# Kernel tuning notes

Measured on AMD Instinct MI355X. Metric: run time of the kernel, lower is better.

## Reference

```python
import jax, jax.numpy as jnp
import numpy as np

N_GROUPS = 32
EPS = 1e-6


def group_norm(x, gamma, beta):
    # x: (b, c, h, w); 32 groups, eps=1e-6, affine
    b, c, h, w = x.shape
    xg = x.reshape(b, N_GROUPS, c // N_GROUPS, h, w)
    mean = xg.mean(axis=(2, 3, 4), keepdims=True)
    var = xg.var(axis=(2, 3, 4), keepdims=True)
    xg = (xg - mean) * jax.lax.rsqrt(var + EPS)
    x = xg.reshape(b, c, h, w)
    return x * gamma[None, :, None, None] + beta[None, :, None, None]


def setup_inputs() -> dict:
    key = jax.random.key(0)
    ks = jax.random.split(key, 8)
    b, c, h, w = 4, 512, 64, 64
    sc = 1.0 / np.sqrt(c)
    return {
        "x": jax.random.normal(ks[0], (b, c, h, w), jnp.float32),
        "gn_w": jnp.ones((c,), jnp.float32),
        "gn_b": jnp.zeros((c,), jnp.float32),
        "wq": jax.random.normal(ks[1], (c, c), jnp.float32) * sc,
        "bq": jnp.zeros((c,), jnp.float32),
        "wk": jax.random.normal(ks[2], (c, c), jnp.float32) * sc,
        "bk": jnp.zeros((c,), jnp.float32),
        "wv": jax.random.normal(ks[3], (c, c), jnp.float32) * sc,
        "bv": jnp.zeros((c,), jnp.float32),
        "wo": jax.random.normal(ks[4], (c, c), jnp.float32) * sc,
        "bo": jnp.zeros((c,), jnp.float32),
    }


def reference(x, gn_w, gn_b, wq, bq, wk, bk, wv, bv, wo, bo):
    b, c, h, w = x.shape
    s = c ** (-0.5)
    xn = group_norm(x, gn_w, gn_b)
    xf = xn.reshape(b, c, h * w)  # (b, c, hw)
    # 1x1 convs == channel matmuls: weight (out_c, in_c)
    q = jnp.einsum('oc,bci->boi', wq, xf) + bq[None, :, None]
    k = jnp.einsum('oc,bci->boi', wk, xf) + bk[None, :, None]
    v = jnp.einsum('oc,bci->boi', wv, xf) + bv[None, :, None]
    attn = jnp.einsum('bci,bcj->bij', q, k) * s  # (b, hw, hw)
    attn = jax.nn.softmax(attn, axis=-1)
    out = jnp.einsum('bij,bcj->bci', attn, v)  # (b, c, hw)
    out = jnp.einsum('oc,bci->boi', wo, out) + bo[None, :, None]
    return out.reshape(b, c, h, w) + x
```

## Files before the change

### kernel.cpp

```cpp
#include <hip/hip_runtime.h>

#define B 4
#define C 512
#define HW 4096
#define NG 32
#define GSZ 65536
#define KROW 528

typedef unsigned short u16;
typedef unsigned int u32;
typedef __attribute__((ext_vector_type(8))) short short8;
typedef __attribute__((ext_vector_type(4))) float f32x4;

__device__ __forceinline__ u16 f2bf(float f) {
    union { u32 i; float f; } x; x.f = f;
    u32 r = x.i + 0x7FFF + ((x.i >> 16) & 1);
    return (u16)(r >> 16);
}
__device__ __forceinline__ u32 cvtpk(float lo, float hi) {
    u32 r;
    asm("v_cvt_pk_bf16_f32 %0, %1, %2" : "=v"(r) : "v"(lo), "v"(hi));
    return r;
}

__device__ __forceinline__ void gld16(const u16* g, u16* l) {
    __builtin_amdgcn_global_load_lds(
        (const __attribute__((address_space(1))) void*)g,
        (__attribute__((address_space(3))) void*)l, 16, 0, 0);
}

__global__ __launch_bounds__(256) void prep_kernel(
        const float* __restrict__ wq, const float* __restrict__ wk,
        const float* __restrict__ wv, const float* __restrict__ wo,
        u16* __restrict__ dst, const float* __restrict__ x,
        float2* __restrict__ part) {
    const int bid = blockIdx.x;
    const int tid = threadIdx.x;
    if (bid < 1024) {
        const int mat = bid >> 8;
        const float* src = (mat == 0) ? wq : (mat == 1) ? wk : (mat == 2) ? wv : wo;
        const int idx = ((bid & 255) * 256 + tid) * 4;
        float4 v = *(const float4*)(src + idx);
        uint2 r = make_uint2(cvtpk(v.x, v.y), cvtpk(v.z, v.w));
        *(uint2*)(dst + (size_t)mat * (C * C) + idx) = r;
        return;
    }
    const int idx2 = bid - 1024;
    const int gl = idx2 >> 2;
    const int qt = idx2 & 3;
    const size_t base = (size_t)gl * GSZ + (size_t)qt * (GSZ / 4);
    float s = 0.f, s2 = 0.f;
    for (int i = tid * 4; i < GSZ / 4; i += 1024) {
        float4 v4 = *(const float4*)(x + base + i);
        s  += v4.x + v4.y + v4.z + v4.w;
        s2 += v4.x*v4.x + v4.y*v4.y + v4.z*v4.z + v4.w*v4.w;
    }
    #pragma unroll
    for (int off = 32; off > 0; off >>= 1) {
        s  += __shfl_down(s, off, 64);
        s2 += __shfl_down(s2, off, 64);
    }
    __shared__ float rs[4], rs2[4];
    int lane = tid & 63, wid = tid >> 6;
    if (lane == 0) { rs[wid] = s; rs2[wid] = s2; }
    __syncthreads();
    if (tid == 0) {
        part[gl * 4 + qt] = make_float2(rs[0] + rs[1] + rs[2] + rs[3],
                                        rs2[0] + rs2[1] + rs2[2] + rs2[3]);
    }
}

__global__ __launch_bounds__(256) void gn_apply_kernel(
        const float* __restrict__ x, const float* __restrict__ gamma,
        const float* __restrict__ beta, const float2* __restrict__ part,
        u16* __restrict__ xnT) {
    const int b = blockIdx.y;
    const int i0 = blockIdx.x * 32;
    const int tid = threadIdx.x;
    __shared__ float gm[512], bt[512];
    __shared__ __align__(16) u16 tile[32 * 512];

    for (int c = tid; c < 512; c += 256) {
        int g = c >> 4;
        const float2* pp = part + ((size_t)b * 32 + g) * 4;
        float2 p0 = pp[0], p1 = pp[1], p2 = pp[2], p3 = pp[3];
        float mean = (p0.x + p1.x + p2.x + p3.x) * (1.f / GSZ);
        float var  = (p0.y + p1.y + p2.y + p3.y) * (1.f / GSZ) - mean * mean;
        float rstd = rsqrtf(var + 1e-6f);
        float gg = gamma[c] * rstd;
        gm[c] = gg;
        bt[c] = beta[c] - mean * gg;
    }
    __syncthreads();
    const int ci = tid >> 5;
    const int ii = tid & 31;
    const float* xb = x + (size_t)b * 512 * 4096 + i0;
    #pragma unroll 4
    for (int p = 0; p < 64; p++) {
        int c = p * 8 + ci;
        float v = xb[(size_t)c * 4096 + ii] * gm[c] + bt[c];
        tile[ii * 512 + (c ^ ((ii & 7) << 3))] = f2bf(v);
    }
    __syncthreads();
    u16* dst = xnT + ((size_t)b * HW + i0) * C;
    #pragma unroll
    for (int p = 0; p < 8; p++) {
        int i = p * 4 + (tid >> 6);
        int ch = tid & 63;
        *(uint4*)(dst + (size_t)i * C + ch * 8) =
            *(const uint4*)&tile[i * 512 + ((ch ^ (i & 7)) << 3)];
    }
}

__global__ __launch_bounds__(256) void qkv_kernel(
        const u16* __restrict__ xnT, const u16* __restrict__ wb,
        const float* __restrict__ bq, const float* __restrict__ bk,
        const float* __restrict__ bv,
        u16* __restrict__ qT, u16* __restrict__ kT, u16* __restrict__ vimg) {
    const int mat = blockIdx.y >> 2;
    const int oT0 = (blockIdx.y & 3) * 128;
    const int iT0 = blockIdx.x * 128;
    const int b = blockIdx.z;
    const u16* Ag = xnT + ((size_t)b * HW + iT0) * C;
    const u16* Bg = wb + (size_t)mat * C * C + (size_t)oT0 * C;
    const float* bias = (mat == 0) ? bq : (mat == 1) ? bk : bv;

    const int tid = threadIdx.x;
    const int w = tid >> 6, lane = tid & 63;
    const int qd = lane >> 4, nn = lane & 15;
    const int wm = w & 1, wn = w >> 1;

    __shared__ __align__(16) u16 smem[16384];
    u16* As0 = smem;
    u16* Bs0 = smem + 8192;

    f32x4 acc[4][4];
    #pragma unroll
    for (int mt = 0; mt < 4; mt++)
        #pragma unroll
        for (int nt = 0; nt < 4; nt++) acc[mt][nt] = (f32x4){0.f, 0.f, 0.f, 0.f};

    auto stage = [&](u16* dst, const u16* g, int c0) {
        #pragma unroll
        for (int p = 0; p < 2; p++) {
            int rbase = 32 * w + 16 * p;
            int row = rbase + (lane >> 2);
            gld16(g + (size_t)row * C + c0 + (((lane & 3) ^ ((row >> 1) & 3)) << 3),
                  dst + rbase * 32);
        }
    };

    stage(As0, Ag, 0);
    stage(Bs0, Bg, 0);

    for (int kt = 0; kt < 16; kt++) {
        const int cur = kt & 1;
        __syncthreads();
        if (kt < 15) {
            stage(As0 + (cur ^ 1) * 4096, Ag, (kt + 1) * 32);
            stage(Bs0 + (cur ^ 1) * 4096, Bg, (kt + 1) * 32);
        }
        const u16* Ac = As0 + cur * 4096;
        const u16* Bc = Bs0 + cur * 4096;
        short8 af[4], bf[4];
        #pragma unroll
        for (int mt = 0; mt < 4; mt++) {
            int row = 64 * wm + 16 * mt + nn;
            af[mt] = *(const short8*)&Ac[row * 32 + ((qd ^ ((row >> 1) & 3)) << 3)];
        }
        #pragma unroll
        for (int nt = 0; nt < 4; nt++) {
            int row = 64 * wn + 16 * nt + nn;
            bf[nt] = *(const short8*)&Bc[row * 32 + ((qd ^ ((row >> 1) & 3)) << 3)];
        }
        #pragma unroll
        for (int mt = 0; mt < 4; mt++)
            #pragma unroll
            for (int nt = 0; nt < 4; nt++)
                acc[mt][nt] = __builtin_amdgcn_mfma_f32_16x16x32_bf16(af[mt], bf[nt], acc[mt][nt], 0, 0, 0);
    }

    __syncthreads();
    u16* dt = smem;

    if (mat < 2) {
        #pragma unroll
        for (int nt = 0; nt < 4; nt++) {
            int o_l = 64 * wn + 16 * nt + nn;
            float bb = bias[oT0 + o_l];
            #pragma unroll
            for (int mt = 0; mt < 4; mt++) {
                int i_l = 64 * wm + 16 * mt + qd * 4;
                dt[(i_l + 0) * 128 + o_l] = f2bf(acc[mt][nt][0] + bb);
                dt[(i_l + 1) * 128 + o_l] = f2bf(acc[mt][nt][1] + bb);
                dt[(i_l + 2) * 128 + o_l] = f2bf(acc[mt][nt][2] + bb);
                dt[(i_l + 3) * 128 + o_l] = f2bf(acc[mt][nt][3] + bb);
            }
        }
        __syncthreads();
        u16* dstT = ((mat == 0) ? qT : kT) + ((size_t)b * HW + iT0) * C + oT0;
        #pragma unroll
        for (int p = 0; p < 8; p++) {
            int i_l = p * 16 + (tid >> 4);
            int ch = tid & 15;
            *(uint4*)(dstT + (size_t)i_l * C + ch * 8) = *(const uint4*)&dt[i_l * 128 + ch * 8];
        }
    } else {
        #pragma unroll
        for (int nt = 0; nt < 4; nt++) {
            int c_l = 64 * wn + 16 * nt + nn;
            float bb = bias[oT0 + c_l];
            #pragma unroll
            for (int mt = 0; mt < 4; mt++) {
                int i_l = 64 * wm + 16 * mt + qd * 4;
                int lc = i_l >> 5;
                int j0 = i_l & 31;
                union { uint2 u; ushort4 s; } st;
                st.u = make_uint2(cvtpk(acc[mt][nt][0] + bb, acc[mt][nt][1] + bb),
                                  cvtpk(acc[mt][nt][2] + bb, acc[mt][nt][3] + bb));
                *(ushort4*)&dt[lc * 4096 + c_l * 32 +
                               (((j0 >> 3) ^ ((c_l >> 2) & 3)) << 3) + (j0 & 7)] = st.s;
            }
        }
        __syncthreads();
        u16* vb = vimg + (size_t)b * 128 * 16384;
        const int chb = iT0 >> 5;
        #pragma unroll
        for (int p = 0; p < 8; p++) {
            int lc = p >> 1, half = p & 1;
            *(uint4*)(vb + (size_t)(chb + lc) * 16384 + oT0 * 32 + half * 2048 + tid * 8) =
                *(const uint4*)&dt[lc * 4096 + half * 2048 + tid * 8];
        }
    }
}

__global__ __launch_bounds__(512, 2) void attn_kernel(
        const u16* __restrict__ qT, const u16* __restrict__ kT,
        const u16* __restrict__ vimg, u16* __restrict__ oT) {
    const int b = blockIdx.y;
    const int i0 = blockIdx.x * 64;
    const int tid = threadIdx.x;
    const int w = tid >> 6;
    const int lane = tid & 63;
    const int q = lane >> 4;
    const int n = lane & 15;
    const int rw = w & 3;
    const int jh = w >> 2;

    __shared__ __align__(16) u16 kbuf[2][32 * KROW];
    __shared__ __align__(16) u16 pbuf[2][64 * 40];
    __shared__ __align__(16) float lpart[2][64];

    short8 qf[16];
    {
        const u16* qrow = qT + ((size_t)b * HW + i0 + rw * 16 + n) * C + q * 8;
        #pragma unroll
        for (int k = 0; k < 16; k++) {
            uint4 u = *(const uint4*)(qrow + k * 32);
            qf[k] = *(const short8*)&u;
        }
    }
    f32x4 oacc[4][4];
    #pragma unroll
    for (int mt = 0; mt < 4; mt++)
        #pragma unroll
        for (int ct = 0; ct < 4; ct++)
            oacc[mt][ct] = (f32x4){0.f, 0.f, 0.f, 0.f};
    float lsum[4] = {0.f, 0.f, 0.f, 0.f};

    const u16* kTb = kT + (size_t)b * HW * C;
    const u16* vTb = vimg + (size_t)b * 128 * 16384;

    auto stageK = [&](int gc, int buf) {
        const u16* gk = kTb + (size_t)gc * 32 * C;
        #pragma unroll
        for (int ii = 0; ii < 4; ii++) {
            int j = w * 4 + ii;
            gld16(gk + (size_t)j * C + ((lane ^ (j & 7)) << 3), &kbuf[buf][j * KROW]);
        }
    };

    const float scale = 0.04419417382415922f;
    stageK(0, 0);
    stageK(1, 1);
    __syncthreads();

    auto s_phase = [&](int slot, int par) {
        f32x4 s0 = {0.f,0.f,0.f,0.f}, s1 = {0.f,0.f,0.f,0.f};
        f32x4 s2 = {0.f,0.f,0.f,0.f}, s3 = {0.f,0.f,0.f,0.f};
        const int sw = n & 7;
        const u16* kb = kbuf[slot] + (jh * 16 + n) * KROW;
        __builtin_amdgcn_s_setprio(1);
        #pragma unroll
        for (int m = 0; m < 4; m++) {
            short8 b0 = *(const short8*)&kb[(((4 * m + 0) * 4 + q) ^ sw) << 3];
            short8 b1 = *(const short8*)&kb[(((4 * m + 1) * 4 + q) ^ sw) << 3];
            short8 b2 = *(const short8*)&kb[(((4 * m + 2) * 4 + q) ^ sw) << 3];
            short8 b3 = *(const short8*)&kb[(((4 * m + 3) * 4 + q) ^ sw) << 3];
            s0 = __builtin_amdgcn_mfma_f32_16x16x32_bf16(qf[4 * m + 0], b0, s0, 0, 0, 0);
            s1 = __builtin_amdgcn_mfma_f32_16x16x32_bf16(qf[4 * m + 1], b1, s1, 0, 0, 0);
            s2 = __builtin_amdgcn_mfma_f32_16x16x32_bf16(qf[4 * m + 2], b2, s2, 0, 0, 0);
            s3 = __builtin_amdgcn_mfma_f32_16x16x32_bf16(qf[4 * m + 3], b3, s3, 0, 0, 0);
        }
        __builtin_amdgcn_s_setprio(0);
        float sv[4];
        #pragma unroll
        for (int r = 0; r < 4; r++) sv[r] = ((s0[r] + s1[r]) + (s2[r] + s3[r])) * scale;
        float p0 = __expf(sv[0]), p1 = __expf(sv[1]);
        float p2 = __expf(sv[2]), p3 = __expf(sv[3]);
        lsum[0] += p0;
        lsum[1] += p1;
        lsum[2] += p2;
        lsum[3] += p3;
        u32 a = cvtpk(p0, p1), c = cvtpk(p2, p3);
        u16* pb = &pbuf[par][(rw * 16 + q * 4) * 40 + jh * 16 + n];
        pb[0]      = (u16)a;
        pb[40]     = (u16)(a >> 16);
        pb[80]     = (u16)c;
        pb[120]    = (u16)(c >> 16);
    };

    s_phase(0, 0);
    __syncthreads();

    #pragma unroll 1
    for (int t = 0; t < 128; ++t) {
        const int cur = t & 1;
        short8 pf[4];
        #pragma unroll
        for (int mt = 0; mt < 4; mt++)
            pf[mt] = *(const short8*)&pbuf[cur][(mt * 16 + n) * 40 + q * 8];
        uint4 vpf[4];
        {
            const u16* gv = vTb + (size_t)t * 16384;
            #pragma unroll
            for (int ct = 0; ct < 4; ct++) {
                int c = w * 64 + ct * 16 + n;
                vpf[ct] = *(const uint4*)&gv[c * 32 + ((q ^ ((c >> 2) & 3)) << 3)];
            }
        }
        if (t < 126) stageK(t + 2, cur);
        if (t < 127) s_phase(cur ^ 1, cur ^ 1);
        __builtin_amdgcn_s_setprio(1);
        #pragma unroll
        for (int ct = 0; ct < 4; ct++) {
            short8 vf = *(const short8*)&vpf[ct];
            #pragma unroll
            for (int mt = 0; mt < 4; mt++)
                oacc[mt][ct] = __builtin_amdgcn_mfma_f32_16x16x32_bf16(pf[mt], vf, oacc[mt][ct], 0, 0, 0);
        }
        __builtin_amdgcn_s_setprio(0);
        __syncthreads();
    }
    #pragma unroll
    for (int r = 0; r < 4; r++) {
        float l = lsum[r];
        l += __shfl_xor(l, 1);
        l += __shfl_xor(l, 2);
        l += __shfl_xor(l, 4);
        l += __shfl_xor(l, 8);
        if (n == 0) lpart[jh][rw * 16 + q * 4 + r] = l;
    }
    __syncthreads();
    #pragma unroll
    for (int mt = 0; mt < 4; mt++) {
        float inv[4];
        #pragma unroll
        for (int r = 0; r < 4; r++) {
            int row = mt * 16 + q * 4 + r;
            inv[r] = 1.f / (lpart[0][row] + lpart[1][row]);
        }
        #pragma unroll
        for (int ct = 0; ct < 4; ct++) {
            int cc = w * 64 + ct * 16 + n;
            size_t base = ((size_t)b * HW + i0 + mt * 16 + q * 4) * C + cc;
            oT[base        ] = f2bf(oacc[mt][ct][0] * inv[0]);
            oT[base +   C  ] = f2bf(oacc[mt][ct][1] * inv[1]);
            oT[base + 2 * C] = f2bf(oacc[mt][ct][2] * inv[2]);
            oT[base + 3 * C] = f2bf(oacc[mt][ct][3] * inv[3]);
        }
    }
}

__global__ __launch_bounds__(256) void proj_kernel(
        const u16* __restrict__ oT, const u16* __restrict__ wob,
        const float* __restrict__ bo, const float* __restrict__ x,
        float* __restrict__ out) {
    const int o0 = blockIdx.y * 128;
    const int i0t = blockIdx.x * 128;
    const int b = blockIdx.z;
    const u16* Ag = wob + (size_t)o0 * C;
    const u16* Bg = oT + ((size_t)b * HW + i0t) * C;

    const int tid = threadIdx.x;
    const int w = tid >> 6, lane = tid & 63;
    const int qd = lane >> 4, nn = lane & 15;
    const int wm = w & 1, wn = w >> 1;

    __shared__ __align__(16) u16 As[2][128 * 32];
    __shared__ __align__(16) u16 Bs[2][128 * 32];

    f32x4 acc[4][4];
    #pragma unroll
    for (int mt = 0; mt < 4; mt++)
        #pragma unroll
        for (int nt = 0; nt < 4; nt++) acc[mt][nt] = (f32x4){0.f, 0.f, 0.f, 0.f};

    auto stage = [&](u16* dst, const u16* g, int c0) {
        #pragma unroll
        for (int p = 0; p < 2; p++) {
            int rbase = 32 * w + 16 * p;
            int row = rbase + (lane >> 2);
            gld16(g + (size_t)row * C + c0 + (((lane & 3) ^ ((row >> 1) & 3)) << 3),
                  dst + rbase * 32);
        }
    };

    stage(As[0], Ag, 0);
    stage(Bs[0], Bg, 0);

    for (int kt = 0; kt < 16; kt++) {
        const int cur = kt & 1;
        __syncthreads();
        if (kt < 15) {
            stage(As[cur ^ 1], Ag, (kt + 1) * 32);
            stage(Bs[cur ^ 1], Bg, (kt + 1) * 32);
        }
        short8 af[4], bf[4];
        #pragma unroll
        for (int mt = 0; mt < 4; mt++) {
            int row = 64 * wm + 16 * mt + nn;
            af[mt] = *(const short8*)&As[cur][row * 32 + ((qd ^ ((row >> 1) & 3)) << 3)];
        }
        #pragma unroll
        for (int nt = 0; nt < 4; nt++) {
            int row = 64 * wn + 16 * nt + nn;
            bf[nt] = *(const short8*)&Bs[cur][row * 32 + ((qd ^ ((row >> 1) & 3)) << 3)];
        }
        #pragma unroll
        for (int mt = 0; mt < 4; mt++)
            #pragma unroll
            for (int nt = 0; nt < 4; nt++)
                acc[mt][nt] = __builtin_amdgcn_mfma_f32_16x16x32_bf16(af[mt], bf[nt], acc[mt][nt], 0, 0, 0);
    }

    #pragma unroll
    for (int mt = 0; mt < 4; mt++) {
        #pragma unroll
        for (int r = 0; r < 4; r++) {
            int o = o0 + 64 * wm + 16 * mt + qd * 4 + r;
            float bb = bo[o];
            #pragma unroll
            for (int nt = 0; nt < 4; nt++) {
                int i = i0t + 64 * wn + 16 * nt + nn;
                size_t idx = ((size_t)b * C + o) * HW + i;
                out[idx] = acc[mt][nt][r] + bb + x[idx];
            }
        }
    }
}

extern "C" void kernel_launch(void* const* d_in, const int* in_sizes, int n_in,
                              void* d_out, int out_size, void* d_ws, size_t ws_size,
                              hipStream_t stream) {
    const float* x    = (const float*)d_in[0];
    const float* gn_w = (const float*)d_in[1];
    const float* gn_b = (const float*)d_in[2];
    const float* wq   = (const float*)d_in[3];
    const float* bq   = (const float*)d_in[4];
    const float* wk   = (const float*)d_in[5];
    const float* bk   = (const float*)d_in[6];
    const float* wv   = (const float*)d_in[7];
    const float* bv   = (const float*)d_in[8];
    const float* wo   = (const float*)d_in[9];
    const float* bo   = (const float*)d_in[10];
    float* out = (float*)d_out;

    const size_t WSZ = (size_t)C * C;
    const size_t S1  = (size_t)B * C * HW;
    u16* wb    = (u16*)d_ws;
    u16* wob   = wb + 3 * WSZ;
    u16* xnT   = wob + WSZ;
    u16* qT    = xnT + S1;
    u16* kT    = qT + S1;
    u16* vimg  = kT + S1;
    u16* oT    = vimg + S1;
    float2* part = (float2*)(oT + S1);

    hipLaunchKernelGGL(prep_kernel,     dim3(1536), dim3(256), 0, stream,
                       wq, wk, wv, wo, wb, x, part);
    hipLaunchKernelGGL(gn_apply_kernel, dim3(HW/32, B), dim3(256), 0, stream,
                       x, gn_w, gn_b, part, xnT);
    hipLaunchKernelGGL(qkv_kernel,      dim3(HW/128, 12, B), dim3(256), 0, stream,
                       xnT, wb, bq, bk, bv, qT, kT, vimg);
    hipLaunchKernelGGL(attn_kernel,     dim3(HW/64, B), dim3(512), 0, stream,
                       qT, kT, vimg, oT);
    hipLaunchKernelGGL(proj_kernel,     dim3(HW/128, C/128, B), dim3(256), 0, stream, oT, wob, bo, x, out);
}
```

Before: 346.4 us.

## Keep softmax probabilities in registers and feed PV via 16x16x16 MFMA

The S MFMA operands are swapped so each lane holds a transposed score tile. That lets the exp'd probabilities be used directly as the A operand of 16x16x16 bf16 MFMAs for the PV product, with only a small register-sized exchange through LDS to fetch the partner half. This replaces the padded LDS P buffer and its re-reads. The V image layout is also changed so the projection writes directly to global in 4-element chunks, with no LDS staging. In exchange, PV now issues twice as many smaller MFMAs and more, narrower V loads per step, and each warp owns 16 rows by 256 channels instead of 64 by 64.

After: 565.4 us. 1.63x slower.

```diff
diff --git a/kernel.cpp b/kernel.cpp
--- a/kernel.cpp
+++ b/kernel.cpp
@@ -11,6 +11,7 @@
 typedef unsigned int u32;
 typedef __attribute__((ext_vector_type(8))) short short8;
 typedef __attribute__((ext_vector_type(4))) float f32x4;
+typedef __attribute__((ext_vector_type(2))) unsigned int u32x2;
 
 __device__ __forceinline__ u16 f2bf(float f) {
     union { u32 i; float f; } x; x.f = f;
@@ -21,6 +22,10 @@
     u32 r;
     asm("v_cvt_pk_bf16_f32 %0, %1, %2" : "=v"(r) : "v"(lo), "v"(hi));
     return r;
+}
+__device__ __forceinline__ f32x4 mfma16(u32x2 a, u32x2 bb, f32x4 c) {
+    asm("v_mfma_f32_16x16x16_bf16 %0, %1, %2, %0" : "+v"(c) : "v"(a), "v"(bb));
+    return c;
 }
 
 __device__ __forceinline__ void gld16(const u16* g, u16* l) {
@@ -206,30 +211,21 @@
             *(uint4*)(dstT + (size_t)i_l * C + ch * 8) = *(const uint4*)&dt[i_l * 128 + ch * 8];
         }
     } else {
+        u16* vb = vimg + (size_t)b * 128 * 16384;
         #pragma unroll
         for (int nt = 0; nt < 4; nt++) {
-            int c_l = 64 * wn + 16 * nt + nn;
-            float bb = bias[oT0 + c_l];
+            int c = oT0 + 64 * wn + 16 * nt + nn;
+            float bb = bias[c];
             #pragma unroll
             for (int mt = 0; mt < 4; mt++) {
-                int i_l = 64 * wm + 16 * mt + qd * 4;
-                int lc = i_l >> 5;
-                int j0 = i_l & 31;
+                int jg = iT0 + 64 * wm + 16 * mt + qd * 4;
+                int ch = jg >> 5;
+                int jq = (jg & 31) >> 2;
                 union { uint2 u; ushort4 s; } st;
                 st.u = make_uint2(cvtpk(acc[mt][nt][0] + bb, acc[mt][nt][1] + bb),
                                   cvtpk(acc[mt][nt][2] + bb, acc[mt][nt][3] + bb));
-                *(ushort4*)&dt[lc * 4096 + c_l * 32 +
-                               (((j0 >> 3) ^ ((c_l >> 2) & 3)) << 3) + (j0 & 7)] = st.s;
+                *(ushort4*)&vb[((size_t)ch * 8 + jq) * 2048 + (size_t)c * 4] = st.s;
             }
-        }
-        __syncthreads();
-        u16* vb = vimg + (size_t)b * 128 * 16384;
-        const int chb = iT0 >> 5;
-        #pragma unroll
-        for (int p = 0; p < 8; p++) {
-            int lc = p >> 1, half = p & 1;
-            *(uint4*)(vb + (size_t)(chb + lc) * 16384 + oT0 * 32 + half * 2048 + tid * 8) =
-                *(const uint4*)&dt[lc * 4096 + half * 2048 + tid * 8];
         }
     }
 }
@@ -248,7 +244,7 @@
     const int jh = w >> 2;
 
     __shared__ __align__(16) u16 kbuf[2][32 * KROW];
-    __shared__ __align__(16) u16 pbuf[2][64 * 40];
+    __shared__ __align__(16) u32x2 pxch[2][8][64];
     __shared__ __align__(16) float lpart[2][64];
 
     short8 qf[16];
@@ -260,13 +256,10 @@
             qf[k] = *(const short8*)&u;
         }
     }
-    f32x4 oacc[4][4];
-    #pragma unroll
-    for (int mt = 0; mt < 4; mt++)
-        #pragma unroll
-        for (int ct = 0; ct < 4; ct++)
-            oacc[mt][ct] = (f32x4){0.f, 0.f, 0.f, 0.f};
-    float lsum[4] = {0.f, 0.f, 0.f, 0.f};
+    f32x4 oacc[16];
+    #pragma unroll
+    for (int ct = 0; ct < 16; ct++) oacc[ct] = (f32x4){0.f, 0.f, 0.f, 0.f};
+    float lsum = 0.f;
 
     const u16* kTb = kT + (size_t)b * HW * C;
     const u16* vTb = vimg + (size_t)b * 128 * 16384;
@@ -285,7 +278,7 @@
     stageK(1, 1);
     __syncthreads();
 
-    auto s_phase = [&](int slot, int par) {
+    auto s_phase = [&](int slot, int par) -> u32x2 {
         f32x4 s0 = {0.f,0.f,0.f,0.f}, s1 = {0.f,0.f,0.f,0.f};
         f32x4 s2 = {0.f,0.f,0.f,0.f}, s3 = {0.f,0.f,0.f,0.f};
         const int sw = n & 7;
@@ -297,10 +290,10 @@
             short8 b1 = *(const short8*)&kb[(((4 * m + 1) * 4 + q) ^ sw) << 3];
             short8 b2 = *(const short8*)&kb[(((4 * m + 2) * 4 + q) ^ sw) << 3];
             short8 b3 = *(const short8*)&kb[(((4 * m + 3) * 4 + q) ^ sw) << 3];
-            s0 = __builtin_amdgcn_mfma_f32_16x16x32_bf16(qf[4 * m + 0], b0, s0, 0, 0, 0);
-            s1 = __builtin_amdgcn_mfma_f32_16x16x32_bf16(qf[4 * m + 1], b1, s1, 0, 0, 0);
-            s2 = __builtin_amdgcn_mfma_f32_16x16x32_bf16(qf[4 * m + 2], b2, s2, 0, 0, 0);
-            s3 = __builtin_amdgcn_mfma_f32_16x16x32_bf16(qf[4 * m + 3], b3, s3, 0, 0, 0);
+            s0 = __builtin_amdgcn_mfma_f32_16x16x32_bf16(b0, qf[4 * m + 0], s0, 0, 0, 0);
+            s1 = __builtin_amdgcn_mfma_f32_16x16x32_bf16(b1, qf[4 * m + 1], s1, 0, 0, 0);
+            s2 = __builtin_amdgcn_mfma_f32_16x16x32_bf16(b2, qf[4 * m + 2], s2, 0, 0, 0);
+            s3 = __builtin_amdgcn_mfma_f32_16x16x32_bf16(b3, qf[4 * m + 3], s3, 0, 0, 0);
         }
         __builtin_amdgcn_s_setprio(0);
         float sv[4];
@@ -308,77 +301,69 @@
         for (int r = 0; r < 4; r++) sv[r] = ((s0[r] + s1[r]) + (s2[r] + s3[r])) * scale;
         float p0 = __expf(sv[0]), p1 = __expf(sv[1]);
         float p2 = __expf(sv[2]), p3 = __expf(sv[3]);
-        lsum[0] += p0;
-        lsum[1] += p1;
-        lsum[2] += p2;
-        lsum[3] += p3;
-        u32 a = cvtpk(p0, p1), c = cvtpk(p2, p3);
-        u16* pb = &pbuf[par][(rw * 16 + q * 4) * 40 + jh * 16 + n];
-        pb[0]      = (u16)a;
-        pb[40]     = (u16)(a >> 16);
-        pb[80]     = (u16)c;
-        pb[120]    = (u16)(c >> 16);
+        lsum += (p0 + p1) + (p2 + p3);
+        u32x2 pq;
+        pq[0] = cvtpk(p0, p1);
+        pq[1] = cvtpk(p2, p3);
+        pxch[par][w][lane] = pq;
+        return pq;
     };
 
-    s_phase(0, 0);
+    u32x2 pA = s_phase(0, 0);
     __syncthreads();
 
     #pragma unroll 1
     for (int t = 0; t < 128; ++t) {
         const int cur = t & 1;
-        short8 pf[4];
-        #pragma unroll
-        for (int mt = 0; mt < 4; mt++)
-            pf[mt] = *(const short8*)&pbuf[cur][(mt * 16 + n) * 40 + q * 8];
-        uint4 vpf[4];
-        {
-            const u16* gv = vTb + (size_t)t * 16384;
-            #pragma unroll
-            for (int ct = 0; ct < 4; ct++) {
-                int c = w * 64 + ct * 16 + n;
-                vpf[ct] = *(const uint4*)&gv[c * 32 + ((q ^ ((c >> 2) & 3)) << 3)];
-            }
+        u32x2 partner = pxch[cur][(jh ^ 1) * 4 + rw][lane];
+        const u16* gv = vTb + (size_t)t * 16384;
+        u32x2 vfo[16];
+        #pragma unroll
+        for (int ct = 0; ct < 16; ct++) {
+            int c = jh * 256 + ct * 16 + n;
+            vfo[ct] = *(const u32x2*)&gv[((jh * 4 + q) * 512 + c) * 4];
         }
         if (t < 126) stageK(t + 2, cur);
-        if (t < 127) s_phase(cur ^ 1, cur ^ 1);
+        u32x2 pB = pA;
+        if (t < 127) pB = s_phase(cur ^ 1, cur ^ 1);
+        u32x2 vfp[16];
+        #pragma unroll
+        for (int ct = 0; ct < 16; ct++) {
+            int c = jh * 256 + ct * 16 + n;
+            vfp[ct] = *(const u32x2*)&gv[(((jh ^ 1) * 4 + q) * 512 + c) * 4];
+        }
         __builtin_amdgcn_s_setprio(1);
         #pragma unroll
-        for (int ct = 0; ct < 4; ct++) {
-            short8 vf = *(const short8*)&vpf[ct];
-            #pragma unroll
-            for (int mt = 0; mt < 4; mt++)
-                oacc[mt][ct] = __builtin_amdgcn_mfma_f32_16x16x32_bf16(pf[mt], vf, oacc[mt][ct], 0, 0, 0);
-        }
+        for (int ct = 0; ct < 16; ct++) oacc[ct] = mfma16(pA, vfo[ct], oacc[ct]);
+        __builtin_amdgcn_s_setprio(0);
+        __builtin_amdgcn_s_setprio(1);
+        #pragma unroll
+        for (int ct = 0; ct < 16; ct++) oacc[ct] = mfma16(partner, vfp[ct], oacc[ct]);
         __builtin_amdgcn_s_setprio(0);
         __syncthreads();
-    }
+        pA = pB;
+    }
+    {
+        float l = lsum;
+        l += __shfl_xor(l, 16);
+        l += __shfl_xor(l, 32);
+        if (q == 0) lpart[jh][rw * 16 + n] = l;
+    }
+    __syncthreads();
+    float inv[4];
     #pragma unroll
     for (int r = 0; r < 4; r++) {
-        float l = lsum[r];
-        l += __shfl_xor(l, 1);
-        l += __shfl_xor(l, 2);
-        l += __shfl_xor(l, 4);
-        l += __shfl_xor(l, 8);
-        if (n == 0) lpart[jh][rw * 16 + q * 4 + r] = l;
-    }
-    __syncthreads();
-    #pragma unroll
-    for (int mt = 0; mt < 4; mt++) {
-        float inv[4];
-        #pragma unroll
-        for (int r = 0; r < 4; r++) {
-            int row = mt * 16 + q * 4 + r;
-            inv[r] = 1.f / (lpart[0][row] + lpart[1][row]);
-        }
-        #pragma unroll
-        for (int ct = 0; ct < 4; ct++) {
-            int cc = w * 64 + ct * 16 + n;
-            size_t base = ((size_t)b * HW + i0 + mt * 16 + q * 4) * C + cc;
-            oT[base        ] = f2bf(oacc[mt][ct][0] * inv[0]);
-            oT[base +   C  ] = f2bf(oacc[mt][ct][1] * inv[1]);
-            oT[base + 2 * C] = f2bf(oacc[mt][ct][2] * inv[2]);
-            oT[base + 3 * C] = f2bf(oacc[mt][ct][3] * inv[3]);
-        }
+        int row = rw * 16 + q * 4 + r;
+        inv[r] = 1.f / (lpart[0][row] + lpart[1][row]);
+    }
+    #pragma unroll
+    for (int ct = 0; ct < 16; ct++) {
+        int c = jh * 256 + ct * 16 + n;
+        size_t base = ((size_t)b * HW + i0 + rw * 16 + q * 4) * C + c;
+        oT[base        ] = f2bf(oacc[ct][0] * inv[0]);
+        oT[base +   C  ] = f2bf(oacc[ct][1] * inv[1]);
+        oT[base + 2 * C] = f2bf(oacc[ct][2] * inv[2]);
+        oT[base + 3 * C] = f2bf(oacc[ct][3] * inv[3]);
     }
 }
 
```
